# Kernel tuning notes

Hardware: AMD Instinct MI355X
Metric: run time of the kernel (lower is better)

The kernel has to match this reference:

```python
import jax, jax.numpy as jnp
import numpy as np

H = 768
NH = 12
DH = H // NH  # 64


def setup_inputs() -> dict:
    key = jax.random.key(0)
    ks = jax.random.split(key, 20)
    s = 1.0 / np.sqrt(H)
    def lin(k, din, dout):
        kw, kb = jax.random.split(k)
        W = jax.random.uniform(kw, (din, dout), jnp.float32, -s, s)
        b = jax.random.uniform(kb, (dout,), jnp.float32, -s, s)
        return W, b
    Wq, bq = lin(ks[0], H, H)
    Wk, bk = lin(ks[1], H, H)
    Wv, bv = lin(ks[2], H, H)
    Wt, bt = lin(ks[3], H, H)
    Wi, bi = lin(ks[4], H, H)
    W1, b1 = lin(ks[5], H, H)
    W2, b2 = lin(ks[6], H, 1)
    text = jax.random.normal(ks[7], (8, 64, H), jnp.float32)
    image = jax.random.normal(ks[8], (8, 197, H), jnp.float32)
    return dict(text=text, image=image, Wq=Wq, bq=bq, Wk=Wk, bk=bk, Wv=Wv, bv=bv,
                Wt=Wt, bt=bt, Wi=Wi, bi=bi, W1=W1, b1=b1, W2=W2, b2=b2)


def reference(text, image, Wq, bq, Wk, bk, Wv, bv, Wt, bt, Wi, bi, W1, b1, W2, b2):
    bsz, t_len, _ = text.shape
    i_len = image.shape[1]
    # relevance gate MLP on broadcast product
    text_emb = text @ Wt + bt          # [b, t, H]
    image_emb = image @ Wi + bi        # [b, i, H]
    rel = text_emb[:, :, None, :] * image_emb[:, None, :, :]  # [b, t, i, H]
    rel = jax.nn.relu(rel @ W1 + b1)
    gate = jax.nn.sigmoid(rel @ W2 + b2)  # [b, t, i, 1]
    gate = gate.reshape(bsz, 1, t_len, i_len)
    # cross-attention
    def heads(x, L):
        return x.reshape(bsz, L, NH, DH).transpose(0, 2, 1, 3)  # [b, h, L, dh]
    q = heads(text @ Wq + bq, t_len)
    k = heads(image @ Wk + bk, i_len)
    v = heads(image @ Wv + bv, i_len)
    scores = jnp.einsum('bhtd,bhid->bhti', q, k) / np.sqrt(DH)
    probs = jax.nn.softmax(scores, axis=-1) * gate   # [b, h, t, i]
    ctx = jnp.einsum('bhti,bhid->bhtd', probs, v)    # [b, h, t, dh]
    return ctx.transpose(0, 2, 1, 3).reshape(bsz, t_len, H)
```

## Files before the change

kernel.cpp:

```cpp
#include <hip/hip_runtime.h>
#include <stdint.h>

#define HD 768
#define NHEADS 12
#define DHEAD 64
#define BATCH 8
#define TLEN 64
#define ILEN 197
#define NPAIRS 100864
#define MTILES 394

typedef __attribute__((ext_vector_type(8))) short short8;
typedef __attribute__((ext_vector_type(4))) float f32x4;

__device__ __forceinline__ short f2bf(float x) {
    union { float f; uint32_t u; } v; v.f = x;
    uint32_t r = v.u + 0x7FFFu + ((v.u >> 16) & 1u);
    return (short)(r >> 16);
}
__device__ __forceinline__ float bf2f(short s) {
    union { uint32_t u; float f; } v; v.u = ((uint32_t)(unsigned short)s) << 16;
    return v.f;
}
__device__ __forceinline__ uint32_t cvtpk(float lo, float hi) {
    uint32_t r;
    asm("v_cvt_pk_bf16_f32 %0, %1, %2" : "=v"(r) : "v"(lo), "v"(hi));
    return r;
}
__device__ __forceinline__ void gll16(const void* g, void* l) {
    __builtin_amdgcn_global_load_lds(
        (const __attribute__((address_space(1))) unsigned int*)g,
        (__attribute__((address_space(3))) unsigned int*)l, 16, 0, 0);
}

__global__ __launch_bounds__(256) void prep_weights(
    const float* __restrict__ Wq, const float* __restrict__ Wk,
    const float* __restrict__ Wv, const float* __restrict__ Wt,
    const float* __restrict__ Wi, const float* __restrict__ W1,
    short* __restrict__ W5s, short* __restrict__ W1Bs)
{
    __shared__ float tile[64][65];
    int bx = blockIdx.x;
    int tid = threadIdx.x;
    if (bx >= 720) {
        int idx = bx - 720;
        int pn = idx / 12, kt = idx - pn * 12;
        int c = tid;
        int j = pn * 256 + c;
        char* chunk = (char*)W1Bs + (size_t)idx * 32768;
        int f = (c >> 1) & 3;
#pragma unroll
        for (int ks = 0; ks < 2; ++ks) {
            char* dst = chunk + ks * 16384 + c * 64;
#pragma unroll
            for (int g = 0; g < 4; ++g) {
                short8 o;
#pragma unroll
                for (int e = 0; e < 8; ++e)
                    o[e] = f2bf(W1[(size_t)(kt * 64 + ks * 32 + g * 8 + e) * HD + j]);
                *(short8*)(dst + ((g * 16) ^ (f << 4))) = o;
            }
        }
        return;
    }
    int seg = bx / 144, ti = bx - seg * 144;
    const float* src = (seg == 0) ? Wt : (seg == 1) ? Wq : (seg == 2) ? Wi
                     : (seg == 3) ? Wk : Wv;
    int kt = ti / 12, ntile = ti - kt * 12;
#pragma unroll
    for (int pass = 0; pass < 16; ++pass) {
        int idx = pass * 256 + tid;
        int kk = idx >> 6, nn = idx & 63;
        tile[kk][nn] = src[(size_t)(kt * 64 + kk) * HD + ntile * 64 + nn];
    }
    __syncthreads();
    size_t base = ((size_t)(seg * 12 + ntile) * 12 + kt) * 8192;
#pragma unroll
    for (int pass = 0; pass < 16; ++pass) {
        int idx = pass * 256 + tid;
        int col = idx >> 6, kloc = idx & 63;
        float x = tile[kloc][col];
        short h = f2bf(x);
        short lw = f2bf(x - bf2f(h));
        int sidx = (col * 64 + kloc) ^ ((col & 7) << 3);
        W5s[base + sidx] = h;
        W5s[base + 4096 + sidx] = lw;
    }
}

__global__ __launch_bounds__(256, 1) void proj_kernel(
    const float* __restrict__ X, int M,
    const short* __restrict__ W5s, int segbase,
    const float* __restrict__ bias0, const float* __restrict__ bias1,
    const float* __restrict__ bias2,
    float* __restrict__ out0, float* __restrict__ out1, float* __restrict__ out2)
{
    __shared__ __align__(16) short Bs[2][8192];
    int tid = threadIdx.x;
    int l = tid & 63, w = tid >> 6;
    int lo = l & 15, grp = l >> 4;
    int y = blockIdx.y;
    int segl = y / 12, ntile = y - segl * 12;
    int seg = segbase + segl;
    const char* wsrc = (const char*)W5s + (size_t)((seg * 12 + ntile) * 12) * 16384;
    {
        const char* s = wsrc + w * 4096 + l * 16;
        char* d = (char*)&Bs[0][0] + w * 4096;
        gll16(s, d); gll16(s + 1024, d + 1024);
        gll16(s + 2048, d + 2048); gll16(s + 3072, d + 3072);
    }
    int arow = blockIdx.x * 64 + w * 16 + lo;
    bool aok = arow < M;
    const float* xrow = X + (size_t)(aok ? arow : 0) * HD;
    short8 ah[24], al[24];
#pragma unroll
    for (int kc = 0; kc < 24; ++kc) {
        int kb = kc * 32 + grp * 8;
        float4 xa = {0.f, 0.f, 0.f, 0.f}, xb = {0.f, 0.f, 0.f, 0.f};
        if (aok) { xa = *(const float4*)(xrow + kb); xb = *(const float4*)(xrow + kb + 4); }
        float xs[8] = {xa.x, xa.y, xa.z, xa.w, xb.x, xb.y, xb.z, xb.w};
#pragma unroll
        for (int e = 0; e < 8; ++e) {
            short hh = f2bf(xs[e]);
            ah[kc][e] = hh;
            al[kc][e] = f2bf(xs[e] - bf2f(hh));
        }
    }
    __syncthreads();

    f32x4 acc[4];
    f32x4 z4 = {0.f, 0.f, 0.f, 0.f};
#pragma unroll
    for (int js = 0; js < 4; ++js) acc[js] = z4;

#pragma unroll
    for (int kk = 0; kk < 12; ++kk) {
        const short* buf = &Bs[kk & 1][0];
        if (kk < 11) {
            const char* s = wsrc + (size_t)(kk + 1) * 16384 + w * 4096 + l * 16;
            char* d = (char*)&Bs[(kk + 1) & 1][0] + w * 4096;
            gll16(s, d); gll16(s + 1024, d + 1024);
            gll16(s + 2048, d + 2048); gll16(s + 3072, d + 3072);
            asm volatile("s_waitcnt vmcnt(4)" ::: "memory");
        } else {
            asm volatile("s_waitcnt vmcnt(0)" ::: "memory");
        }
        __builtin_amdgcn_s_barrier();
        asm volatile("" ::: "memory");
#pragma unroll
        for (int js = 0; js < 4; ++js) {
            int col = js * 16 + lo;
            int base = col * 64;
            int sw = (col & 7) << 3;
#pragma unroll
            for (int kcl = 0; kcl < 2; ++kcl) {
                int idx = (base + kcl * 32 + grp * 8) ^ sw;
                short8 bh = *(const short8*)&buf[idx];
                short8 bl = *(const short8*)&buf[4096 + idx];
                int kc = kk * 2 + kcl;
                acc[js] = __builtin_amdgcn_mfma_f32_16x16x32_bf16(ah[kc], bh, acc[js], 0, 0, 0);
                acc[js] = __builtin_amdgcn_mfma_f32_16x16x32_bf16(ah[kc], bl, acc[js], 0, 0, 0);
                acc[js] = __builtin_amdgcn_mfma_f32_16x16x32_bf16(al[kc], bh, acc[js], 0, 0, 0);
            }
        }
        asm volatile("s_waitcnt lgkmcnt(0)" ::: "memory");
        __builtin_amdgcn_s_barrier();
        asm volatile("" ::: "memory");
    }
    const float* bp = (segl == 0) ? bias0 : (segl == 1) ? bias1 : bias2;
    float* op = (segl == 0) ? out0 : (segl == 1) ? out1 : out2;
#pragma unroll
    for (int js = 0; js < 4; ++js) {
        int cc = ntile * 64 + js * 16 + lo;
        float bvv = bp[cc];
#pragma unroll
        for (int r = 0; r < 4; ++r) {
            int orow = blockIdx.x * 64 + w * 16 + grp * 4 + r;
            if (orow < M) op[(size_t)orow * HD + cc] = acc[js][r] + bvv;
        }
    }
}

__global__ __launch_bounds__(512, 1) void gate_gemm(
    const float* __restrict__ te, const float* __restrict__ ie,
    const short* __restrict__ W1Bs, const float* __restrict__ b1,
    const float* __restrict__ W2, float* __restrict__ plg)
{
    __shared__ __align__(16) char lds[131072];
    __shared__ float te_s[3 * HD];
    __shared__ int ieoff[256];
    int tid = threadIdx.x;
    int lane = tid & 63, wid = tid >> 6;
    int lo = lane & 15, grp = lane >> 4;
    int wr = wid >> 2, wc = wid & 3;
    int bx0 = blockIdx.x;
    int nwg = gridDim.x;
    int qq = nwg >> 3, rr8 = nwg & 7;
    int xcd = bx0 & 7;
    int logical = (xcd < rr8 ? xcd * (qq + 1) : rr8 * (qq + 1) + (xcd - rr8) * qq)
                + (bx0 >> 3);
    int m_l = logical / 3, pn = logical - m_l * 3;

    const char* Bg = (const char*)W1Bs + (size_t)pn * 12 * 32768;
    int bt0 = (m_l * 256) / 197;

    if (tid < 256) {
        int p = m_l * 256 + tid;
        int bt = p / 197;
        int i = p - bt * 197;
        int b = bt >> 6;
        ieoff[tid] = (b * 197 + i) * HD | ((bt - bt0) << 24);
    }
    for (int idx = tid; idx < 3 * HD; idx += 512) {
        int r = idx / HD;
        int bt = bt0 + r; if (bt > 511) bt = 511;
        te_s[idx] = te[(size_t)bt * HD + (idx - r * HD)];
    }
    __syncthreads();

    auto constructA0 = [&](int t, int par) {
#pragma unroll
        for (int u = 0; u < 8; ++u) {
            int w = u * 512 + tid;
            int row = w >> 4, f4 = w & 15;
            int pk = ieoff[row];
            float4 x = *(const float4*)(ie + (pk & 0xFFFFFF) + t * 64 + f4 * 4);
            const float* tp = &te_s[(pk >> 24) * HD + t * 64 + f4 * 4];
            float4 tv = *(const float4*)tp;
            uint32_t o0 = cvtpk(x.x * tv.x, x.y * tv.y);
            uint32_t o1 = cvtpk(x.z * tv.z, x.w * tv.w);
            int ks = f4 >> 3, r7 = f4 & 7, g = r7 >> 1, half = r7 & 1;
            char* dst = lds + par * 32768 + ks * 16384 + row * 64
                      + ((g * 16) ^ (((row >> 1) & 3) << 4)) + half * 8;
            uint2 o = {o0, o1};
            *(uint2*)dst = o;
        }
    };
    constructA0(0, 0);
    {
        const char* s = Bg + tid * 16;
        char* d = lds + 65536 + tid * 16;
        gll16(s, d); gll16(s + 8192, d + 8192);
        gll16(s + 16384, d + 16384); gll16(s + 24576, d + 24576);
    }
    asm volatile("s_waitcnt vmcnt(0) lgkmcnt(0)" ::: "memory");
    __builtin_amdgcn_s_barrier();
    asm volatile("" ::: "memory");

    f32x4 acc[8][4];
    f32x4 z4 = {0.f, 0.f, 0.f, 0.f};
#pragma unroll
    for (int rt = 0; rt < 8; ++rt)
#pragma unroll
        for (int ct = 0; ct < 4; ++ct) acc[rt][ct] = z4;

    for (int kt = 0; kt < 12; ++kt) {
        int par = kt & 1, npar = par ^ 1;
        int aoff = par * 32768;
        int boff = 65536 + par * 32768;
        bool more = kt < 11;

        float4 xi[8];
        if (more) {
#pragma unroll
            for (int u = 0; u < 8; ++u) {
                int w = u * 512 + tid;
                int row = w >> 4, f4 = w & 15;
                int pk = ieoff[row];
                xi[u] = *(const float4*)(ie + (pk & 0xFFFFFF) + (kt + 1) * 64 + f4 * 4);
            }
            const char* s = Bg + (size_t)(kt + 1) * 32768 + tid * 16;
            char* d = lds + 65536 + npar * 32768 + tid * 16;
            gll16(s, d); gll16(s + 8192, d + 8192);
            gll16(s + 16384, d + 16384); gll16(s + 24576, d + 24576);
        }

        short8 bfr[4], af[4];
#pragma unroll
        for (int ph = 0; ph < 4; ++ph) {
            int ksp = ph >> 1;
            int rh  = ph & 1;
            if (rh == 0) {
#pragma unroll
                for (int ct = 0; ct < 4; ++ct) {
                    int c = wc * 64 + ct * 16 + lo;
                    bfr[ct] = *(const short8*)(lds + boff + ksp * 16384 + c * 64
                                + ((grp * 16) ^ (((c >> 1) & 3) << 4)));
                }
            }
#pragma unroll
            for (int j = 0; j < 4; ++j) {
                int r = wr * 128 + (rh * 4 + j) * 16 + lo;
                af[j] = *(const short8*)(lds + aoff + ksp * 16384 + r * 64
                            + ((grp * 16) ^ (((r >> 1) & 3) << 4)));
            }
            __builtin_amdgcn_s_barrier();
            asm volatile("s_waitcnt lgkmcnt(0)" ::: "memory");
            __builtin_amdgcn_sched_barrier(0);
            __builtin_amdgcn_s_setprio(1);
#pragma unroll
            for (int j = 0; j < 4; ++j)
#pragma unroll
                for (int ct = 0; ct < 4; ++ct)
                    acc[rh * 4 + j][ct] = __builtin_amdgcn_mfma_f32_16x16x32_bf16(
                        af[j], bfr[ct], acc[rh * 4 + j][ct], 0, 0, 0);
            __builtin_amdgcn_s_setprio(0);
            if (ph < 3) {
                __builtin_amdgcn_s_barrier();
                asm volatile("" ::: "memory");
            }
        }

        if (more) {
            asm volatile("s_waitcnt vmcnt(0)" ::: "memory");
#pragma unroll
            for (int u = 0; u < 8; ++u) {
                int w = u * 512 + tid;
                int row = w >> 4, f4 = w & 15;
                int pk = ieoff[row];
                const float* tp = &te_s[(pk >> 24) * HD + (kt + 1) * 64 + f4 * 4];
                float4 tv = *(const float4*)tp;
                float4 x = xi[u];
                uint32_t o0 = cvtpk(x.x * tv.x, x.y * tv.y);
                uint32_t o1 = cvtpk(x.z * tv.z, x.w * tv.w);
                int ks = f4 >> 3, r7 = f4 & 7, g = r7 >> 1, half = r7 & 1;
                char* dst = lds + npar * 32768 + ks * 16384 + row * 64
                          + ((g * 16) ^ (((row >> 1) & 3) << 4)) + half * 8;
                uint2 o = {o0, o1};
                *(uint2*)dst = o;
            }
        } else {
            asm volatile("s_waitcnt vmcnt(0)" ::: "memory");
        }
        asm volatile("s_waitcnt lgkmcnt(0)" ::: "memory");
        __builtin_amdgcn_s_barrier();
        asm volatile("" ::: "memory");
    }

    float b1v[4], w2v[4];
#pragma unroll
    for (int ct = 0; ct < 4; ++ct) {
        int j = pn * 256 + wc * 64 + ct * 16 + lo;
        b1v[ct] = b1[j]; w2v[ct] = W2[j];
    }
    float pl[8][4];
#pragma unroll
    for (int rt = 0; rt < 8; ++rt)
#pragma unroll
        for (int r = 0; r < 4; ++r) {
            float s = 0.f;
#pragma unroll
            for (int ct = 0; ct < 4; ++ct)
                s += fmaxf(acc[rt][ct][r] + b1v[ct], 0.f) * w2v[ct];
            pl[rt][r] = s;
        }
#pragma unroll
    for (int msk = 1; msk <= 8; msk <<= 1)
#pragma unroll
        for (int rt = 0; rt < 8; ++rt)
#pragma unroll
            for (int r = 0; r < 4; ++r)
                pl[rt][r] += __shfl_xor(pl[rt][r], msk);

    __syncthreads();
    float* red = (float*)lds;
    if (lo == 0) {
#pragma unroll
        for (int rt = 0; rt < 8; ++rt)
#pragma unroll
            for (int r = 0; r < 4; ++r)
                red[wid * 128 + rt * 16 + grp * 4 + r] = pl[rt][r];
    }
    __syncthreads();
    if (tid < 256) {
        int wr_ = tid >> 7, rl = tid & 127;
        float s = red[(wr_ * 4 + 0) * 128 + rl] + red[(wr_ * 4 + 1) * 128 + rl]
                + red[(wr_ * 4 + 2) * 128 + rl] + red[(wr_ * 4 + 3) * 128 + rl];
        plg[(size_t)pn * NPAIRS + (size_t)m_l * 256 + tid] = s;
    }
}

__global__ __launch_bounds__(256) void gate_fin(
    const float* __restrict__ plg, const float* __restrict__ b2,
    float* __restrict__ gateb)
{
    int idx = blockIdx.x * 256 + threadIdx.x;
    if (idx < NPAIRS) {
        float s = plg[idx] + plg[NPAIRS + idx] + plg[2 * NPAIRS + idx] + b2[0];
        gateb[idx] = 1.f / (1.f + __expf(-s));
    }
}

__global__ __launch_bounds__(256) void attn_kernel(
    const float* __restrict__ q, const float* __restrict__ k,
    const float* __restrict__ v, const float* __restrict__ gate,
    float* __restrict__ out)
{
    __shared__ float k_s[ILEN * 65];
    __shared__ float p_s[4][ILEN][4];
    int bx = blockIdx.x;
    int tq = bx & 3;
    int h = (bx >> 2) % NHEADS;
    int b = bx / (4 * NHEADS);
    int tid = threadIdx.x;
    for (int idx = tid; idx < ILEN * DHEAD; idx += 256) {
        int i = idx >> 6, d = idx & 63;
        k_s[i * 65 + d] = k[(size_t)(b * ILEN + i) * HD + h * DHEAD + d];
    }
    __syncthreads();

    int l = tid & 63, w = tid >> 6;
    int tbase = tq * 16 + w * 4;

    for (int tt = 0; tt < 4; ++tt) {
        int t = tbase + tt;
        float qv = q[(size_t)(b * 64 + t) * HD + h * DHEAD + l];
        float s0 = 0.f, s1 = 0.f, s2 = 0.f, s3 = 0.f;
        int i0 = l, i1 = 64 + l, i2 = 128 + l;
        int i3c = (192 + l < ILEN) ? 192 + l : 0;
        for (int d = 0; d < 64; ++d) {
            float qd = __shfl(qv, d);
            s0 += qd * k_s[i0 * 65 + d];
            s1 += qd * k_s[i1 * 65 + d];
            s2 += qd * k_s[i2 * 65 + d];
            s3 += qd * k_s[i3c * 65 + d];
        }
        float sc[4] = {s0, s1, s2, s3};
        float m = -3.0e38f;
#pragma unroll
        for (int rep = 0; rep < 4; ++rep) {
            int i = rep * 64 + l;
            sc[rep] = (i < ILEN) ? sc[rep] * 0.125f : -3.0e38f;
            m = fmaxf(m, sc[rep]);
        }
        for (int mask = 32; mask >= 1; mask >>= 1) m = fmaxf(m, __shfl_xor(m, mask));
        float sum = 0.f;
#pragma unroll
        for (int rep = 0; rep < 4; ++rep) {
            float e = __expf(sc[rep] - m);
            sc[rep] = e;
            sum += e;
        }
        for (int mask = 32; mask >= 1; mask >>= 1) sum += __shfl_xor(sum, mask);
        float inv = 1.f / sum;
        const float* grow = gate + (size_t)(b * 64 + t) * ILEN;
#pragma unroll
        for (int rep = 0; rep < 4; ++rep) {
            int i = rep * 64 + l;
            if (i < ILEN) p_s[w][i][tt] = sc[rep] * inv * grow[i];
        }
    }

    float ctx[4] = {0.f, 0.f, 0.f, 0.f};
    const float* vbase = v + (size_t)(b * ILEN) * HD + h * DHEAD + l;
#pragma unroll 4
    for (int i = 0; i < ILEN; ++i) {
        float vv = vbase[(size_t)i * HD];
        float4 p4 = *(const float4*)&p_s[w][i][0];
        ctx[0] += p4.x * vv;
        ctx[1] += p4.y * vv;
        ctx[2] += p4.z * vv;
        ctx[3] += p4.w * vv;
    }
#pragma unroll
    for (int tt = 0; tt < 4; ++tt)
        out[(size_t)(b * 64 + tbase + tt) * HD + h * DHEAD + l] = ctx[tt];
}

extern "C" void kernel_launch(void* const* d_in, const int* in_sizes, int n_in,
                              void* d_out, int out_size, void* d_ws, size_t ws_size,
                              hipStream_t stream)
{
    const float* text  = (const float*)d_in[0];
    const float* image = (const float*)d_in[1];
    const float* Wq = (const float*)d_in[2];
    const float* bq = (const float*)d_in[3];
    const float* Wk = (const float*)d_in[4];
    const float* bk = (const float*)d_in[5];
    const float* Wv = (const float*)d_in[6];
    const float* bv = (const float*)d_in[7];
    const float* Wt = (const float*)d_in[8];
    const float* bt = (const float*)d_in[9];
    const float* Wi = (const float*)d_in[10];
    const float* bi = (const float*)d_in[11];
    const float* W1 = (const float*)d_in[12];
    const float* b1 = (const float*)d_in[13];
    const float* W2 = (const float*)d_in[14];
    const float* b2 = (const float*)d_in[15];
    float* out = (float*)d_out;

    char* ws = (char*)d_ws;
    size_t off = 0;
    auto carve = [&](size_t bytes) -> void* {
        void* p = (void*)(ws + off);
        off += (bytes + 255) & ~(size_t)255;
        return p;
    };
    short* W5s  = (short*)carve((size_t)5 * 144 * 8192 * 2);
    short* W1Bs = (short*)carve((size_t)36 * 32768);
    float* te    = (float*)carve((size_t)512 * 768 * 4);
    float* qb    = (float*)carve((size_t)512 * 768 * 4);
    float* ieb   = (float*)carve((size_t)1576 * 768 * 4);
    float* kb    = (float*)carve((size_t)1576 * 768 * 4);
    float* vb    = (float*)carve((size_t)1576 * 768 * 4);
    float* gateb = (float*)carve((size_t)NPAIRS * 4);
    float* plg   = (float*)carve((size_t)3 * NPAIRS * 4);

    hipLaunchKernelGGL(prep_weights, dim3(756), dim3(256), 0, stream,
                       Wq, Wk, Wv, Wt, Wi, W1, W5s, W1Bs);
    hipLaunchKernelGGL(proj_kernel, dim3(8, 24), dim3(256), 0, stream,
                       text, 512, W5s, 0, bt, bq, (const float*)nullptr,
                       te, qb, (float*)nullptr);
    hipLaunchKernelGGL(proj_kernel, dim3(25, 36), dim3(256), 0, stream,
                       image, 1576, W5s, 2, bi, bk, bv,
                       ieb, kb, vb);
    hipLaunchKernelGGL(gate_gemm, dim3(MTILES * 3), dim3(512), 0, stream,
                       te, ieb, W1Bs, b1, W2, plg);
    hipLaunchKernelGGL(gate_fin, dim3((NPAIRS + 255) / 256), dim3(256), 0, stream,
                       plg, b2, gateb);
    hipLaunchKernelGGL(attn_kernel, dim3(BATCH * NHEADS * 4), dim3(256), 0, stream,
                       qb, kb, vb, gateb, out);
}
```

Baseline: 336.0 us.

## Interleave next-tile A construction with MFMA phases using staged vmcnt waits

The conversion and LDS store of the next K-tile's A operand (image×text product packed to bf16) is split into four pairs of units. Each pair now runs right after one of the four MFMA phases, instead of all eight running in one block after the MFMA loop. The global loads for the next tile are issued after the B-tile async copies and guarded by sched_barriers. Graduated s_waitcnt vmcnt values then let each phase wait only for the loads it needs. This aims to hide global load latency and the conversion ALU work behind matrix-core execution. The cost is more reliance on exact in-order vmcnt accounting and tighter register pressure.

```diff
diff --git a/kernel.cpp b/kernel.cpp
--- a/kernel.cpp
+++ b/kernel.cpp
@@ -218,26 +218,29 @@
     }
     __syncthreads();
 
-    auto constructA0 = [&](int t, int par) {
+    auto constructUnit = [&](int t, int par, int u, float4 x) {
+        int w = u * 512 + tid;
+        int row = w >> 4, f4 = w & 15;
+        int pk = ieoff[row];
+        const float* tp = &te_s[(pk >> 24) * HD + t * 64 + f4 * 4];
+        float4 tv = *(const float4*)tp;
+        uint32_t o0 = cvtpk(x.x * tv.x, x.y * tv.y);
+        uint32_t o1 = cvtpk(x.z * tv.z, x.w * tv.w);
+        int ks = f4 >> 3, r7 = f4 & 7, g = r7 >> 1, half = r7 & 1;
+        char* dst = lds + par * 32768 + ks * 16384 + row * 64
+                  + ((g * 16) ^ (((row >> 1) & 3) << 4)) + half * 8;
+        uint2 o = {o0, o1};
+        *(uint2*)dst = o;
+    };
+    {
 #pragma unroll
         for (int u = 0; u < 8; ++u) {
             int w = u * 512 + tid;
             int row = w >> 4, f4 = w & 15;
             int pk = ieoff[row];
-            float4 x = *(const float4*)(ie + (pk & 0xFFFFFF) + t * 64 + f4 * 4);
-            const float* tp = &te_s[(pk >> 24) * HD + t * 64 + f4 * 4];
-            float4 tv = *(const float4*)tp;
-            uint32_t o0 = cvtpk(x.x * tv.x, x.y * tv.y);
-            uint32_t o1 = cvtpk(x.z * tv.z, x.w * tv.w);
-            int ks = f4 >> 3, r7 = f4 & 7, g = r7 >> 1, half = r7 & 1;
-            char* dst = lds + par * 32768 + ks * 16384 + row * 64
-                      + ((g * 16) ^ (((row >> 1) & 3) << 4)) + half * 8;
-            uint2 o = {o0, o1};
-            *(uint2*)dst = o;
-        }
-    };
-    constructA0(0, 0);
-    {
+            float4 x = *(const float4*)(ie + (pk & 0xFFFFFF) + f4 * 4);
+            constructUnit(0, 0, u, x);
+        }
         const char* s = Bg + tid * 16;
         char* d = lds + 65536 + tid * 16;
         gll16(s, d); gll16(s + 8192, d + 8192);
@@ -262,17 +265,23 @@
 
         float4 xi[8];
         if (more) {
-#pragma unroll
-            for (int u = 0; u < 8; ++u) {
-                int w = u * 512 + tid;
-                int row = w >> 4, f4 = w & 15;
-                int pk = ieoff[row];
-                xi[u] = *(const float4*)(ie + (pk & 0xFFFFFF) + (kt + 1) * 64 + f4 * 4);
-            }
             const char* s = Bg + (size_t)(kt + 1) * 32768 + tid * 16;
             char* d = lds + 65536 + npar * 32768 + tid * 16;
             gll16(s, d); gll16(s + 8192, d + 8192);
             gll16(s + 16384, d + 16384); gll16(s + 24576, d + 24576);
+            __builtin_amdgcn_sched_barrier(0);
+#pragma unroll
+            for (int pair = 0; pair < 4; ++pair) {
+#pragma unroll
+                for (int q = 0; q < 2; ++q) {
+                    int u = pair * 2 + q;
+                    int w = u * 512 + tid;
+                    int row = w >> 4, f4 = w & 15;
+                    int pk = ieoff[row];
+                    xi[u] = *(const float4*)(ie + (pk & 0xFFFFFF) + (kt + 1) * 64 + f4 * 4);
+                }
+                __builtin_amdgcn_sched_barrier(0);
+            }
         }
 
         short8 bfr[4], af[4];
@@ -305,36 +314,21 @@
                     acc[rh * 4 + j][ct] = __builtin_amdgcn_mfma_f32_16x16x32_bf16(
                         af[j], bfr[ct], acc[rh * 4 + j][ct], 0, 0, 0);
             __builtin_amdgcn_s_setprio(0);
-            if (ph < 3) {
-                __builtin_amdgcn_s_barrier();
-                asm volatile("" ::: "memory");
+            if (more) {
+                if (ph == 0)      asm volatile("s_waitcnt vmcnt(6)" ::: "memory");
+                else if (ph == 1) asm volatile("s_waitcnt vmcnt(4)" ::: "memory");
+                else if (ph == 2) asm volatile("s_waitcnt vmcnt(2)" ::: "memory");
+                else              asm volatile("s_waitcnt vmcnt(0)" ::: "memory");
+                constructUnit(kt + 1, npar, ph * 2,     xi[ph * 2]);
+                constructUnit(kt + 1, npar, ph * 2 + 1, xi[ph * 2 + 1]);
+            } else if (ph == 3) {
+                asm volatile("s_waitcnt vmcnt(0)" ::: "memory");
             }
-        }
-
-        if (more) {
-            asm volatile("s_waitcnt vmcnt(0)" ::: "memory");
-#pragma unroll
-            for (int u = 0; u < 8; ++u) {
-                int w = u * 512 + tid;
-                int row = w >> 4, f4 = w & 15;
-                int pk = ieoff[row];
-                const float* tp = &te_s[(pk >> 24) * HD + (kt + 1) * 64 + f4 * 4];
-                float4 tv = *(const float4*)tp;
-                float4 x = xi[u];
-                uint32_t o0 = cvtpk(x.x * tv.x, x.y * tv.y);
-                uint32_t o1 = cvtpk(x.z * tv.z, x.w * tv.w);
-                int ks = f4 >> 3, r7 = f4 & 7, g = r7 >> 1, half = r7 & 1;
-                char* dst = lds + npar * 32768 + ks * 16384 + row * 64
-                          + ((g * 16) ^ (((row >> 1) & 3) << 4)) + half * 8;
-                uint2 o = {o0, o1};
-                *(uint2*)dst = o;
-            }
-        } else {
-            asm volatile("s_waitcnt vmcnt(0)" ::: "memory");
-        }
-        asm volatile("s_waitcnt lgkmcnt(0)" ::: "memory");
-        __builtin_amdgcn_s_barrier();
-        asm volatile("" ::: "memory");
+            if (ph == 3)
+                asm volatile("s_waitcnt lgkmcnt(0)" ::: "memory");
+            __builtin_amdgcn_s_barrier();
+            asm volatile("" ::: "memory");
+        }
     }
 
     float b1v[4], w2v[4];
```

After: 335.4 us. About the same (-0.2%).
